# Kernel tuning notes

Measured on AMD Instinct MI355X. Metric: run time of the kernel, lower is better.

## Reference

```python
import jax, jax.numpy as jnp
import numpy as np

BIG = 1e9
EPS_BETA = 1e-6
EPS_BN = 1e-5

N_NODES = 50000
N_EDGES = 800000
IN_DIM = 128
OUT_DIM = 128


def setup_inputs() -> dict:
    key = jax.random.key(0)
    ks = jax.random.split(key, 8)
    h = jax.random.normal(ks[0], (N_NODES, IN_DIM), dtype=jnp.float32)
    src = jax.random.randint(ks[1], (N_EDGES,), 0, N_NODES, dtype=jnp.int32)
    dst = jax.random.randint(ks[2], (N_EDGES,), 0, N_NODES, dtype=jnp.int32)
    sigma_GD = jax.random.uniform(ks[3], (N_EDGES,), dtype=jnp.float32)
    fc_w = jax.random.normal(ks[4], (IN_DIM, OUT_DIM), dtype=jnp.float32) / np.sqrt(IN_DIM)
    fc_b = jax.random.normal(ks[5], (OUT_DIM,), dtype=jnp.float32) * 0.01
    attn_w = jax.random.normal(ks[6], (2 * OUT_DIM, 1), dtype=jnp.float32) / np.sqrt(2 * OUT_DIM)
    attn_b = jax.random.normal(ks[7], (1,), dtype=jnp.float32) * 0.01
    bn_gamma = jnp.ones((OUT_DIM,), dtype=jnp.float32)
    bn_beta = jnp.zeros((OUT_DIM,), dtype=jnp.float32)
    return {"h": h, "src": src, "dst": dst, "sigma_GD": sigma_GD,
            "fc_w": fc_w, "fc_b": fc_b, "attn_w": attn_w, "attn_b": attn_b,
            "bn_gamma": bn_gamma, "bn_beta": bn_beta}


def reference(h, src, dst, sigma_GD, fc_w, fc_b, attn_w, attn_b, bn_gamma, bn_beta):
    n = h.shape[0]
    # node projection
    z = h @ fc_w + fc_b                                   # [N, D]
    z = jnp.where(jnp.isinf(z), BIG, z)
    # per-edge attention logits: concat(src,dst) @ W == src@W1 + dst@W2 (avoid concat materialization)
    d = z.shape[1]
    w_src, w_dst = attn_w[:d], attn_w[d:]
    z_src = z[src]                                        # [E, D]
    a = z_src @ w_src + z[dst] @ w_dst + attn_b           # [E, 1]
    a = jnp.where(jnp.isinf(a), BIG, a)
    e = jax.nn.leaky_relu(a, negative_slope=0.01)[:, 0]   # [E]
    # segment softmax over incoming edges (mailbox softmax)
    m = jax.ops.segment_max(e, dst, num_segments=n)       # [N]
    ex = jnp.exp(e - m[dst])
    denom = jax.ops.segment_sum(ex, dst, num_segments=n)  # [N]
    alpha = ex / denom[dst]                               # [E]
    # beta: sigma_GD normalized per destination node
    bsum = jax.ops.segment_sum(sigma_GD, dst, num_segments=n)
    beta = sigma_GD / (bsum[dst] + EPS_BETA)              # [E]
    # weighted scatter-sum of source features
    h_new = jax.ops.segment_sum((alpha * beta)[:, None] * z_src, dst, num_segments=n)  # [N, D]
    h_new = jnp.where(jnp.isinf(h_new), BIG, h_new)
    # BatchNorm1d (training-mode batch stats, biased variance, as torch does)
    mu = h_new.mean(axis=0)
    var = ((h_new - mu) ** 2).mean(axis=0)
    h_bn = (h_new - mu) * jax.lax.rsqrt(var + EPS_BN) * bn_gamma + bn_beta
    return jax.nn.elu(h_bn)
```

## Files before the change

kernel.cpp:

```cpp
#include <hip/hip_runtime.h>
#include <hip/hip_fp16.h>
#include <math.h>

#define N_NODES 50000
#define N_EDGES 800000
#define BIGV 1000000000.0f
#define NBLK_GEMM 3125
#define CHUNK 1024
#define NCHUNK 782
#define NCH4 784
#define NBUCKET 1563
#define NBK4 1564
#define BMAX 768
#define OVFSTRIDE 1024
#define NBLK_BN 512

typedef _Float16 half8 __attribute__((ext_vector_type(8)));
typedef float floatx4 __attribute__((ext_vector_type(4)));

__device__ __forceinline__ float clampinf(float x) { return isinf(x) ? BIGV : x; }

__device__ __forceinline__ void barrier_lgkm_only() {
    __builtin_amdgcn_sched_barrier(0);
    asm volatile("s_waitcnt lgkmcnt(0)" ::: "memory");
    __builtin_amdgcn_s_barrier();
    __builtin_amdgcn_sched_barrier(0);
}

__global__ __launch_bounds__(256) void k_prep(const float* __restrict__ W,
                                              __half* __restrict__ wt,
                                              float* __restrict__ bns,
                                              const int* __restrict__ dst,
                                              int* __restrict__ countsT)
{
    __shared__ int hist[NBK4];
    const int t = threadIdx.x;
    const int idx = blockIdx.x * 256 + t;
    if (idx < 16384) {
        int n = idx >> 7, k = idx & 127;
        wt[idx] = __float2half(W[k * 128 + n]);
    }
    if (idx < 256) bns[idx] = 0.f;
    for (int i = t; i < NBK4; i += 256) hist[i] = 0;
    __syncthreads();
    const int base = blockIdx.x * CHUNK;
    for (int i = t; i < CHUNK; i += 256) {
        int e = base + i;
        if (e < N_EDGES) atomicAdd(&hist[dst[e] >> 5], 1);
    }
    __syncthreads();
    for (int i = t; i < NBK4; i += 256)
        countsT[(size_t)i * NCH4 + blockIdx.x] = hist[i];
}

__global__ __launch_bounds__(256) void k_off(const int* __restrict__ countsT,
                                             int* __restrict__ cursC,
                                             int* __restrict__ btot)
{
    const int wv = (blockIdx.x << 2) + (threadIdx.x >> 6);
    const int l = threadIdx.x & 63;
    if (wv >= NBUCKET) {
        if (l == 0 && wv < NBK4) btot[wv] = 0;
        return;
    }
    const int* row = countsT + (size_t)wv * NCH4;
    int carry = 0;
    #pragma unroll
    for (int p = 0; p < 13; ++p) {
        const int c = p * 64 + l;
        const int v = (c < NCHUNK) ? row[c] : 0;
        int x = v;
        #pragma unroll
        for (int o = 1; o < 64; o <<= 1) {
            int u = __shfl_up(x, o);
            if (l >= o) x += u;
        }
        if (c < NCHUNK) cursC[(size_t)c * NBK4 + wv] = carry + x - v;
        carry += __shfl(x, 63);
    }
    if (l == 0) btot[wv] = carry;
}

__global__ __launch_bounds__(256) void k_gemm(
    const float* __restrict__ h, const __half* __restrict__ wt,
    const float* __restrict__ bias, const float* __restrict__ attn_w,
    __half* __restrict__ zh, float* __restrict__ sv, float* __restrict__ tv)
{
    __shared__ _Float16 hA[16][136];
    __shared__ float spart[4][16], tpart[4][16];

    const int tid = threadIdx.x;
    const int lane = tid & 63;
    const int wv = tid >> 6;
    const int l16 = lane & 15;
    const int oct = lane >> 4;
    const int n0 = wv << 5;
    const int node0 = blockIdx.x << 4;

    {
        const float4* h4 = (const float4*)(h + (size_t)node0 * 128);
        for (int i = tid; i < 512; i += 256) {
            int r = i >> 5, c4 = i & 31;
            float4 v = h4[i];
            union { __half2 h2[2]; uint2 u; } pk;
            pk.h2[0] = __floats2half2_rn(v.x, v.y);
            pk.h2[1] = __floats2half2_rn(v.z, v.w);
            *(uint2*)&hA[r][c4 << 2] = pk.u;
        }
    }

    half8 bfrag[4][2];
    #pragma unroll
    for (int kk = 0; kk < 4; ++kk)
        #pragma unroll
        for (int t = 0; t < 2; ++t)
            bfrag[kk][t] = *(const half8*)(wt + (size_t)(n0 + t * 16 + l16) * 128
                                              + kk * 32 + oct * 8);

    const float bv0 = bias[n0 + l16],         bv1 = bias[n0 + 16 + l16];
    const float ws0 = attn_w[n0 + l16],       ws1 = attn_w[n0 + 16 + l16];
    const float wd0 = attn_w[128 + n0 + l16], wd1 = attn_w[128 + n0 + 16 + l16];

    barrier_lgkm_only();

    floatx4 acc0 = {0.f, 0.f, 0.f, 0.f};
    floatx4 acc1 = {0.f, 0.f, 0.f, 0.f};
    #pragma unroll
    for (int kk = 0; kk < 4; ++kk) {
        half8 a = *(const half8*)&hA[l16][(kk << 5) + (oct << 3)];
        acc0 = __builtin_amdgcn_mfma_f32_16x16x32_f16(a, bfrag[kk][0], acc0, 0, 0, 0);
        acc1 = __builtin_amdgcn_mfma_f32_16x16x32_f16(a, bfrag[kk][1], acc1, 0, 0, 0);
    }

    float s_acc[4], t_acc[4];
    #pragma unroll
    for (int r = 0; r < 4; ++r) {
        float z0 = clampinf(acc0[r] + bv0);
        float z1 = clampinf(acc1[r] + bv1);
        const int row = (oct << 2) + r;
        zh[(size_t)(node0 + row) * 128 + n0 + l16]      = __float2half(z0);
        zh[(size_t)(node0 + row) * 128 + n0 + 16 + l16] = __float2half(z1);
        s_acc[r] = z0 * ws0 + z1 * ws1;
        t_acc[r] = z0 * wd0 + z1 * wd1;
    }
    #pragma unroll
    for (int r = 0; r < 4; ++r) {
        #pragma unroll
        for (int o = 1; o < 16; o <<= 1) {
            s_acc[r] += __shfl_xor(s_acc[r], o);
            t_acc[r] += __shfl_xor(t_acc[r], o);
        }
    }
    if (l16 == 0) {
        #pragma unroll
        for (int r = 0; r < 4; ++r) {
            spart[wv][(oct << 2) + r] = s_acc[r];
            tpart[wv][(oct << 2) + r] = t_acc[r];
        }
    }
    barrier_lgkm_only();
    if (tid < 16) {
        sv[node0 + tid] = spart[0][tid] + spart[1][tid] + spart[2][tid] + spart[3][tid];
        tv[node0 + tid] = tpart[0][tid] + tpart[1][tid] + tpart[2][tid] + tpart[3][tid];
    }
}

__global__ __launch_bounds__(512) void k_scat(
    const int* __restrict__ src, const int* __restrict__ dst,
    const float* __restrict__ sigma,
    const float* __restrict__ sv, const float* __restrict__ tv,
    const float* __restrict__ attn_b,
    const int* __restrict__ cursC, const int* __restrict__ btot,
    float4* __restrict__ tmp, int* __restrict__ bbase_g)
{
    __shared__ int cur[NBK4];
    __shared__ int bb[NBK4];
    __shared__ int tsc[512];
    const int t = threadIdx.x;
    const int self = blockIdx.x;

    for (int i = t; i < NBK4; i += 512) cur[i] = cursC[(size_t)self * NBK4 + i];

    uint4 bt = {0u, 0u, 0u, 0u};
    int tsum = 0;
    if (t < NBK4 / 4) {
        bt = ((const uint4*)btot)[t];
        tsum = (int)(bt.x + bt.y + bt.z + bt.w);
    }
    tsc[t] = tsum;
    __syncthreads();
    for (int off = 1; off < 512; off <<= 1) {
        int u = (t >= off) ? tsc[t - off] : 0;
        __syncthreads();
        tsc[t] += u;
        __syncthreads();
    }
    if (t < NBK4 / 4) {
        const int v0 = tsc[t] - tsum;
        bb[4*t+0] = v0;
        bb[4*t+1] = v0 + (int)bt.x;
        bb[4*t+2] = v0 + (int)bt.x + (int)bt.y;
        bb[4*t+3] = v0 + (int)bt.x + (int)bt.y + (int)bt.z;
    }
    __syncthreads();
    for (int i = t; i < NBK4; i += 512) cur[i] += bb[i];
    if (self == 0)
        for (int i = t; i < NBK4; i += 512) bbase_g[i] = bb[i];
    __syncthreads();

    const float ab = attn_b[0];
    const int base = self * CHUNK;
    for (int i = t; i < CHUNK; i += 512) {
        int e = base + i;
        if (e < N_EDGES) {
            int s = src[e];
            int d = dst[e];
            float a = sv[s] + tv[d] + ab;
            a = clampinf(a);
            float ev = a > 0.f ? a : 0.01f * a;
            int pos = atomicAdd(&cur[d >> 5], 1);
            float4 rec;
            rec.x = __int_as_float(s);
            rec.y = sigma[e];
            rec.z = ev;
            rec.w = __int_as_float(d);
            tmp[pos] = rec;
        }
    }
}

__global__ __launch_bounds__(512) void k_bagg(
    const float4* __restrict__ tmp, const int* __restrict__ bbase_g,
    const __half* __restrict__ zh, float4* __restrict__ ovf,
    float* __restrict__ out)
{
    __shared__ float4 lrec[BMAX];
    __shared__ int hist[32];
    __shared__ int segs[33];
    __shared__ int cur[32];
    const int t = threadIdx.x;
    const int b = blockIdx.x;
    const int s0 = bbase_g[b];
    const int n  = bbase_g[b + 1] - s0;

    if (t < 32) hist[t] = 0;
    __syncthreads();
    const float* tw = (const float*)tmp;
    for (int i = t; i < n; i += 512) {
        int d = __float_as_int(tw[4 * (size_t)(s0 + i) + 3]);
        atomicAdd(&hist[d & 31], 1);
    }
    __syncthreads();
    if (t < 32) {
        const int hv = hist[t];
        int x = hv;
        #pragma unroll
        for (int o = 1; o < 32; o <<= 1) {
            int u = __shfl_up(x, o);
            if (t >= o) x += u;
        }
        segs[t] = x - hv;
        cur[t]  = x - hv;
        if (t == 31) segs[32] = x;
    }
    __syncthreads();
    for (int i = t; i < n; i += 512) {
        float4 rec = tmp[s0 + i];
        int d = __float_as_int(rec.w);
        int pos = atomicAdd(&cur[d & 31], 1);
        if (pos < BMAX) lrec[pos] = rec;
        else            ovf[(size_t)b * OVFSTRIDE + (pos - BMAX)] = rec;
    }
    __syncthreads();

    const int lane = t & 63;
    const int wv = t >> 6;
    const int grp = lane >> 4;
    const int l16 = lane & 15;

    for (int j = wv; j < 32; j += 8) {
        const int node = (b << 5) + j;
        if (node >= N_NODES) continue;
        const int beg = segs[j];
        const int deg = segs[j + 1] - beg;
        float acc[8] = {0.f,0.f,0.f,0.f,0.f,0.f,0.f,0.f};

        if (deg > 0) {
            if (deg <= 64 && n <= BMAX) {
                int sidx = 0; float sig = 0.f, e = -INFINITY;
                if (lane < deg) {
                    float4 r = lrec[beg + lane];
                    sidx = __float_as_int(r.x); sig = r.y; e = r.z;
                }
                float m = e;
                for (int o = 32; o; o >>= 1) m = fmaxf(m, __shfl_xor(m, o));
                float p = (lane < deg) ? __expf(e - m) : 0.f;
                float dn = p, bs = sig;
                for (int o = 32; o; o >>= 1) {
                    dn += __shfl_xor(dn, o);
                    bs += __shfl_xor(bs, o);
                }
                const float coef = p * sig * (1.0f / dn) / (bs + 1e-6f);
                if (lane < deg) lrec[beg + lane].y = coef;
                const int dm = deg - 1;
                for (int c = 0; c < deg; c += 16) {
                    const int j0 = c + grp, j1 = j0 + 4, j2 = j0 + 8, j3 = j0 + 12;
                    float2 q0 = *(const float2*)&lrec[beg + min(j0, dm)];
                    float2 q1 = *(const float2*)&lrec[beg + min(j1, dm)];
                    float2 q2 = *(const float2*)&lrec[beg + min(j2, dm)];
                    float2 q3 = *(const float2*)&lrec[beg + min(j3, dm)];
                    uint4 r0 = *(const uint4*)(zh + ((size_t)__float_as_int(q0.x) << 7) + (l16 << 3));
                    uint4 r1 = *(const uint4*)(zh + ((size_t)__float_as_int(q1.x) << 7) + (l16 << 3));
                    uint4 r2 = *(const uint4*)(zh + ((size_t)__float_as_int(q2.x) << 7) + (l16 << 3));
                    uint4 r3 = *(const uint4*)(zh + ((size_t)__float_as_int(q3.x) << 7) + (l16 << 3));
                    const float c0 = (j0 < deg) ? q0.y : 0.f;
                    const float c1 = (j1 < deg) ? q1.y : 0.f;
                    const float c2 = (j2 < deg) ? q2.y : 0.f;
                    const float c3 = (j3 < deg) ? q3.y : 0.f;
                    const __half2* h0 = (const __half2*)&r0;
                    const __half2* h1 = (const __half2*)&r1;
                    const __half2* h2 = (const __half2*)&r2;
                    const __half2* h3 = (const __half2*)&r3;
                    #pragma unroll
                    for (int k = 0; k < 4; ++k) {
                        float2 f0 = __half22float2(h0[k]);
                        float2 f1 = __half22float2(h1[k]);
                        float2 f2 = __half22float2(h2[k]);
                        float2 f3 = __half22float2(h3[k]);
                        acc[2*k]   = fmaf(c0, f0.x, acc[2*k]);
                        acc[2*k+1] = fmaf(c0, f0.y, acc[2*k+1]);
                        acc[2*k]   = fmaf(c1, f1.x, acc[2*k]);
                        acc[2*k+1] = fmaf(c1, f1.y, acc[2*k+1]);
                        acc[2*k]   = fmaf(c2, f2.x, acc[2*k]);
                        acc[2*k+1] = fmaf(c2, f2.y, acc[2*k+1]);
                        acc[2*k]   = fmaf(c3, f3.x, acc[2*k]);
                        acc[2*k+1] = fmaf(c3, f3.y, acc[2*k+1]);
                    }
                }
            } else if (deg <= 64) {
                int sidx = 0; float sig = 0.f, e = -INFINITY;
                if (lane < deg) {
                    const int off = beg + lane;
                    float4 r = (off < BMAX) ? lrec[off]
                             : ovf[(size_t)b * OVFSTRIDE + (off - BMAX)];
                    sidx = __float_as_int(r.x); sig = r.y; e = r.z;
                }
                float m = e;
                for (int o = 32; o; o >>= 1) m = fmaxf(m, __shfl_xor(m, o));
                float p = (lane < deg) ? __expf(e - m) : 0.f;
                float dn = p, bs = sig;
                for (int o = 32; o; o >>= 1) {
                    dn += __shfl_xor(dn, o);
                    bs += __shfl_xor(bs, o);
                }
                const float coef = p * sig * (1.0f / dn) / (bs + 1e-6f);
                for (int c = 0; c < deg; c += 4) {
                    const int jj = c + grp;
                    const int js = (jj < deg) ? jj : 0;
                    float cf = __shfl(coef, js);
                    int sj = __shfl(sidx, js);
                    if (jj < deg) {
                        uint4 raw = *(const uint4*)(zh + ((size_t)sj << 7) + (l16 << 3));
                        const __half2* hp = (const __half2*)&raw;
                        #pragma unroll
                        for (int k = 0; k < 4; ++k) {
                            float2 f = __half22float2(hp[k]);
                            acc[2*k]   = fmaf(cf, f.x, acc[2*k]);
                            acc[2*k+1] = fmaf(cf, f.y, acc[2*k+1]);
                        }
                    }
                }
            } else {
                float m = -INFINITY;
                for (int i = lane; i < deg; i += 64) {
                    const int off = beg + i;
                    float4 r = (off < BMAX) ? lrec[off]
                             : ovf[(size_t)b * OVFSTRIDE + (off - BMAX)];
                    m = fmaxf(m, r.z);
                }
                for (int o = 32; o; o >>= 1) m = fmaxf(m, __shfl_xor(m, o));
                float dn = 0.f, bs = 0.f;
                for (int i = lane; i < deg; i += 64) {
                    const int off = beg + i;
                    float4 r = (off < BMAX) ? lrec[off]
                             : ovf[(size_t)b * OVFSTRIDE + (off - BMAX)];
                    dn += __expf(r.z - m); bs += r.y;
                }
                for (int o = 32; o; o >>= 1) {
                    dn += __shfl_xor(dn, o);
                    bs += __shfl_xor(bs, o);
                }
                const float scale = (1.0f / dn) / (bs + 1e-6f);
                for (int c = 0; c < deg; c += 64) {
                    int i = c + lane;
                    int sidx = 0; float coef = 0.f;
                    if (i < deg) {
                        const int off = beg + i;
                        float4 r = (off < BMAX) ? lrec[off]
                                 : ovf[(size_t)b * OVFSTRIDE + (off - BMAX)];
                        sidx = __float_as_int(r.x);
                        coef = __expf(r.z - m) * r.y * scale;
                    }
                    const int cnt2 = min(64, deg - c);
                    for (int jj = 0; jj < cnt2; jj += 4) {
                        const int j4 = jj + grp;
                        const int js = (j4 < cnt2) ? j4 : 0;
                        float cf = __shfl(coef, js);
                        int sj = __shfl(sidx, js);
                        if (j4 < cnt2) {
                            uint4 raw = *(const uint4*)(zh + ((size_t)sj << 7) + (l16 << 3));
                            const __half2* hp = (const __half2*)&raw;
                            #pragma unroll
                            for (int k = 0; k < 4; ++k) {
                                float2 f = __half22float2(hp[k]);
                                acc[2*k]   = fmaf(cf, f.x, acc[2*k]);
                                acc[2*k+1] = fmaf(cf, f.y, acc[2*k+1]);
                            }
                        }
                    }
                }
            }
        }
        #pragma unroll
        for (int k = 0; k < 8; ++k) {
            acc[k] += __shfl_xor(acc[k], 16);
            acc[k] += __shfl_xor(acc[k], 32);
        }
        if (grp == 0) {
            float4 o0, o1;
            o0.x = clampinf(acc[0]); o0.y = clampinf(acc[1]);
            o0.z = clampinf(acc[2]); o0.w = clampinf(acc[3]);
            o1.x = clampinf(acc[4]); o1.y = clampinf(acc[5]);
            o1.z = clampinf(acc[6]); o1.w = clampinf(acc[7]);
            float4* op = (float4*)(out + (size_t)node * 128 + (l16 << 3));
            op[0] = o0; op[1] = o1;
        }
    }
}

__global__ __launch_bounds__(256) void k_bnstats(const float* __restrict__ hnew,
                                                 float* __restrict__ partials)
{
    const int tid = threadIdx.x;
    const int f4 = (tid & 31) << 2;
    const int rgrp = tid >> 5;
    float4 s = {0.f, 0.f, 0.f, 0.f}, q = {0.f, 0.f, 0.f, 0.f};
    for (int node = blockIdx.x * 8 + rgrp; node < N_NODES; node += NBLK_BN * 8) {
        float4 v = *(const float4*)(hnew + (size_t)node * 128 + f4);
        s.x += v.x; s.y += v.y; s.z += v.z; s.w += v.w;
        q.x += v.x * v.x; q.y += v.y * v.y; q.z += v.z * v.z; q.w += v.w * v.w;
    }
    __shared__ float4 ls[256], lq[256];
    ls[tid] = s; lq[tid] = q;
    __syncthreads();
    for (int off = 128; off >= 32; off >>= 1) {
        if (tid < off) {
            float4 a = ls[tid + off], b = lq[tid + off];
            ls[tid].x += a.x; ls[tid].y += a.y; ls[tid].z += a.z; ls[tid].w += a.w;
            lq[tid].x += b.x; lq[tid].y += b.y; lq[tid].z += b.z; lq[tid].w += b.w;
        }
        __syncthreads();
    }
    if (tid < 32) {
        float* p = partials + (size_t)blockIdx.x * 256;
        *(float4*)(p + f4)       = ls[tid];
        *(float4*)(p + 128 + f4) = lq[tid];
    }
}

__global__ __launch_bounds__(1024) void k_bnred(const float* __restrict__ partials,
                                                float* __restrict__ sums)
{
    __shared__ float red[4][256];
    const int t = threadIdx.x;
    const int f = t & 255;
    const int part = t >> 8;
    float s = 0.f;
    #pragma unroll 8
    for (int b = part * (NBLK_BN / 4); b < (part + 1) * (NBLK_BN / 4); ++b)
        s += partials[(size_t)b * 256 + f];
    red[part][f] = s;
    __syncthreads();
    if (part == 0)
        sums[f] = red[0][f] + red[1][f] + red[2][f] + red[3][f];
}

__global__ __launch_bounds__(256) void k_bnapply(float* __restrict__ io,
                                                 const float* __restrict__ sums,
                                                 const float* __restrict__ gamma,
                                                 const float* __restrict__ beta)
{
    __shared__ float sc[128], sh[128];
    const int tid = threadIdx.x;
    if (tid < 128) {
        const float invn = 1.0f / (float)N_NODES;
        float mu = sums[tid] * invn;
        float var = fmaxf(sums[128 + tid] * invn - mu * mu, 0.f);
        float g = gamma[tid] * rsqrtf(var + 1e-5f);
        sc[tid] = g;
        sh[tid] = beta[tid] - mu * g;
    }
    __syncthreads();
    const size_t idx = (size_t)blockIdx.x * 256 + tid;
    const int f4 = ((int)idx & 31) << 2;
    float4 x = ((const float4*)io)[idx];
    float y0 = x.x * sc[f4 + 0] + sh[f4 + 0];
    float y1 = x.y * sc[f4 + 1] + sh[f4 + 1];
    float y2 = x.z * sc[f4 + 2] + sh[f4 + 2];
    float y3 = x.w * sc[f4 + 3] + sh[f4 + 3];
    float4 o;
    o.x = y0 > 0.f ? y0 : expm1f(y0);
    o.y = y1 > 0.f ? y1 : expm1f(y1);
    o.z = y2 > 0.f ? y2 : expm1f(y2);
    o.w = y3 > 0.f ? y3 : expm1f(y3);
    ((float4*)io)[idx] = o;
}

extern "C" void kernel_launch(void* const* d_in, const int* in_sizes, int n_in,
                              void* d_out, int out_size, void* d_ws, size_t ws_size,
                              hipStream_t stream)
{
    const float* h      = (const float*)d_in[0];
    const int*   src    = (const int*)  d_in[1];
    const int*   dst    = (const int*)  d_in[2];
    const float* sigma  = (const float*)d_in[3];
    const float* fc_w   = (const float*)d_in[4];
    const float* fc_b   = (const float*)d_in[5];
    const float* attn_w = (const float*)d_in[6];
    const float* attn_b = (const float*)d_in[7];
    const float* gamma  = (const float*)d_in[8];
    const float* beta   = (const float*)d_in[9];
    float* out = (float*)d_out;

    float4* tmp    = (float4*)d_ws;
    float4* ovf    = tmp + N_EDGES;
    __half* zh     = (__half*)(ovf + (size_t)NBK4 * OVFSTRIDE);
    float*  sv     = (float*)(zh + (size_t)N_NODES * 128);
    float*  tv     = sv + N_NODES;
    float*  bns    = tv + N_NODES;
    float*  parts  = bns + 256;
    __half* wt     = (__half*)(parts + (size_t)NBLK_BN * 256);
    int*    countsT= (int*)(wt + 16384);
    int*    cursC  = countsT + (size_t)NBK4 * NCH4;
    int*    btot   = cursC + (size_t)NCH4 * NBK4;
    int*    bbase  = btot + NBK4;

    k_prep    <<<NCHUNK, 256, 0, stream>>>(fc_w, wt, bns, dst, countsT);
    k_off     <<<NBK4 / 4, 256, 0, stream>>>(countsT, cursC, btot);
    k_gemm    <<<NBLK_GEMM, 256, 0, stream>>>(h, wt, fc_b, attn_w, zh, sv, tv);
    k_scat    <<<NCHUNK, 512, 0, stream>>>(src, dst, sigma, sv, tv, attn_b,
                                           cursC, btot, tmp, bbase);
    k_bagg    <<<NBUCKET, 512, 0, stream>>>(tmp, bbase, zh, ovf, out);
    k_bnstats <<<NBLK_BN, 256, 0, stream>>>(out, parts);
    k_bnred   <<<1, 1024, 0, stream>>>(parts, bns);
    k_bnapply <<<(N_NODES * 128) / (256 * 4), 256, 0, stream>>>(out, bns, gamma, beta);
}
```

Measured before the change: 218.1 us.

## Compute per-node softmax stats with block-wide LDS atomics during bucket scatter

Records are now read once into registers, reused for both the histogram and the scatter pass, which drops the second global read. During the scatter, per-node max (via an ordered int key) and sigma sums are accumulated with LDS atomics. A new block-wide pass computes the exponentials, the denominators and a per-node scale. The per-wave shuffle reductions in the common fast path are removed, and the fast path no longer requires deg<=64. The cost is more LDS atomics and extra barriers, and float atomic summation order becomes nondeterministic.

Result: faster. 208.6 us (-4.4%).

```diff
diff --git a/kernel.cpp b/kernel.cpp
--- a/kernel.cpp
+++ b/kernel.cpp
@@ -19,6 +19,14 @@
 typedef float floatx4 __attribute__((ext_vector_type(4)));
 
 __device__ __forceinline__ float clampinf(float x) { return isinf(x) ? BIGV : x; }
+
+__device__ __forceinline__ int fkey(float x) {
+    int b = __float_as_int(x);
+    return (b >= 0) ? b : (b ^ 0x7FFFFFFF);
+}
+__device__ __forceinline__ float fkey_inv(int k) {
+    return __int_as_float((k >= 0) ? k : (k ^ 0x7FFFFFFF));
+}
 
 __device__ __forceinline__ void barrier_lgkm_only() {
     __builtin_amdgcn_sched_barrier(0);
@@ -238,18 +246,27 @@
     __shared__ int hist[32];
     __shared__ int segs[33];
     __shared__ int cur[32];
+    __shared__ int mkey[32];
+    __shared__ float dnod[32], bsum[32], scale[32];
     const int t = threadIdx.x;
     const int b = blockIdx.x;
     const int s0 = bbase_g[b];
     const int n  = bbase_g[b + 1] - s0;
 
-    if (t < 32) hist[t] = 0;
-    __syncthreads();
-    const float* tw = (const float*)tmp;
-    for (int i = t; i < n; i += 512) {
-        int d = __float_as_int(tw[4 * (size_t)(s0 + i) + 3]);
-        atomicAdd(&hist[d & 31], 1);
-    }
+    if (t < 32) {
+        hist[t] = 0; mkey[t] = (int)0x80000000;
+        dnod[t] = 0.f; bsum[t] = 0.f;
+    }
+    __syncthreads();
+
+    float4 rec0, rec1;
+    const bool h0 = (t < n), h1 = (t + 512 < n);
+    if (h0) rec0 = tmp[s0 + t];
+    if (h1) rec1 = tmp[s0 + t + 512];
+    if (h0) atomicAdd(&hist[__float_as_int(rec0.w) & 31], 1);
+    if (h1) atomicAdd(&hist[__float_as_int(rec1.w) & 31], 1);
+    for (int i = t + 1024; i < n; i += 512)
+        atomicAdd(&hist[__float_as_int(tmp[s0 + i].w) & 31], 1);
     __syncthreads();
     if (t < 32) {
         const int hv = hist[t];
@@ -264,13 +281,44 @@
         if (t == 31) segs[32] = x;
     }
     __syncthreads();
-    for (int i = t; i < n; i += 512) {
+    if (h0) {
+        const int bin = __float_as_int(rec0.w) & 31;
+        int pos = atomicAdd(&cur[bin], 1);
+        if (pos < BMAX) lrec[pos] = rec0;
+        else            ovf[(size_t)b * OVFSTRIDE + (pos - BMAX)] = rec0;
+        atomicAdd(&bsum[bin], rec0.y);
+        atomicMax(&mkey[bin], fkey(rec0.z));
+    }
+    if (h1) {
+        const int bin = __float_as_int(rec1.w) & 31;
+        int pos = atomicAdd(&cur[bin], 1);
+        if (pos < BMAX) lrec[pos] = rec1;
+        else            ovf[(size_t)b * OVFSTRIDE + (pos - BMAX)] = rec1;
+        atomicAdd(&bsum[bin], rec1.y);
+        atomicMax(&mkey[bin], fkey(rec1.z));
+    }
+    for (int i = t + 1024; i < n; i += 512) {
         float4 rec = tmp[s0 + i];
-        int d = __float_as_int(rec.w);
-        int pos = atomicAdd(&cur[d & 31], 1);
+        const int bin = __float_as_int(rec.w) & 31;
+        int pos = atomicAdd(&cur[bin], 1);
         if (pos < BMAX) lrec[pos] = rec;
         else            ovf[(size_t)b * OVFSTRIDE + (pos - BMAX)] = rec;
-    }
+        atomicAdd(&bsum[bin], rec.y);
+        atomicMax(&mkey[bin], fkey(rec.z));
+    }
+    __syncthreads();
+    if (n <= BMAX) {
+        for (int i = t; i < n; i += 512) {
+            float4 r = lrec[i];
+            const int bin = __float_as_int(r.w) & 31;
+            const float m = fkey_inv(mkey[bin]);
+            const float p = __expf(r.z - m);
+            atomicAdd(&dnod[bin], p);
+            lrec[i].w = p * r.y;
+        }
+    }
+    __syncthreads();
+    if (t < 32) scale[t] = (1.0f / dnod[t]) / (bsum[t] + 1e-6f);
     __syncthreads();
 
     const int lane = t & 63;
@@ -286,47 +334,33 @@
         float acc[8] = {0.f,0.f,0.f,0.f,0.f,0.f,0.f,0.f};
 
         if (deg > 0) {
-            if (deg <= 64 && n <= BMAX) {
-                int sidx = 0; float sig = 0.f, e = -INFINITY;
-                if (lane < deg) {
-                    float4 r = lrec[beg + lane];
-                    sidx = __float_as_int(r.x); sig = r.y; e = r.z;
-                }
-                float m = e;
-                for (int o = 32; o; o >>= 1) m = fmaxf(m, __shfl_xor(m, o));
-                float p = (lane < deg) ? __expf(e - m) : 0.f;
-                float dn = p, bs = sig;
-                for (int o = 32; o; o >>= 1) {
-                    dn += __shfl_xor(dn, o);
-                    bs += __shfl_xor(bs, o);
-                }
-                const float coef = p * sig * (1.0f / dn) / (bs + 1e-6f);
-                if (lane < deg) lrec[beg + lane].y = coef;
+            if (n <= BMAX) {
+                const float sc = scale[j];
                 const int dm = deg - 1;
                 for (int c = 0; c < deg; c += 16) {
                     const int j0 = c + grp, j1 = j0 + 4, j2 = j0 + 8, j3 = j0 + 12;
-                    float2 q0 = *(const float2*)&lrec[beg + min(j0, dm)];
-                    float2 q1 = *(const float2*)&lrec[beg + min(j1, dm)];
-                    float2 q2 = *(const float2*)&lrec[beg + min(j2, dm)];
-                    float2 q3 = *(const float2*)&lrec[beg + min(j3, dm)];
+                    float4 q0 = lrec[beg + min(j0, dm)];
+                    float4 q1 = lrec[beg + min(j1, dm)];
+                    float4 q2 = lrec[beg + min(j2, dm)];
+                    float4 q3 = lrec[beg + min(j3, dm)];
                     uint4 r0 = *(const uint4*)(zh + ((size_t)__float_as_int(q0.x) << 7) + (l16 << 3));
                     uint4 r1 = *(const uint4*)(zh + ((size_t)__float_as_int(q1.x) << 7) + (l16 << 3));
                     uint4 r2 = *(const uint4*)(zh + ((size_t)__float_as_int(q2.x) << 7) + (l16 << 3));
                     uint4 r3 = *(const uint4*)(zh + ((size_t)__float_as_int(q3.x) << 7) + (l16 << 3));
-                    const float c0 = (j0 < deg) ? q0.y : 0.f;
-                    const float c1 = (j1 < deg) ? q1.y : 0.f;
-                    const float c2 = (j2 < deg) ? q2.y : 0.f;
-                    const float c3 = (j3 < deg) ? q3.y : 0.f;
-                    const __half2* h0 = (const __half2*)&r0;
-                    const __half2* h1 = (const __half2*)&r1;
-                    const __half2* h2 = (const __half2*)&r2;
-                    const __half2* h3 = (const __half2*)&r3;
+                    const float c0 = (j0 < deg) ? q0.w * sc : 0.f;
+                    const float c1 = (j1 < deg) ? q1.w * sc : 0.f;
+                    const float c2 = (j2 < deg) ? q2.w * sc : 0.f;
+                    const float c3 = (j3 < deg) ? q3.w * sc : 0.f;
+                    const __half2* h0p = (const __half2*)&r0;
+                    const __half2* h1p = (const __half2*)&r1;
+                    const __half2* h2p = (const __half2*)&r2;
+                    const __half2* h3p = (const __half2*)&r3;
                     #pragma unroll
                     for (int k = 0; k < 4; ++k) {
-                        float2 f0 = __half22float2(h0[k]);
-                        float2 f1 = __half22float2(h1[k]);
-                        float2 f2 = __half22float2(h2[k]);
-                        float2 f3 = __half22float2(h3[k]);
+                        float2 f0 = __half22float2(h0p[k]);
+                        float2 f1 = __half22float2(h1p[k]);
+                        float2 f2 = __half22float2(h2p[k]);
+                        float2 f3 = __half22float2(h3p[k]);
                         acc[2*k]   = fmaf(c0, f0.x, acc[2*k]);
                         acc[2*k+1] = fmaf(c0, f0.y, acc[2*k+1]);
                         acc[2*k]   = fmaf(c1, f1.x, acc[2*k]);
@@ -390,7 +424,7 @@
                     dn += __shfl_xor(dn, o);
                     bs += __shfl_xor(bs, o);
                 }
-                const float scale = (1.0f / dn) / (bs + 1e-6f);
+                const float scl = (1.0f / dn) / (bs + 1e-6f);
                 for (int c = 0; c < deg; c += 64) {
                     int i = c + lane;
                     int sidx = 0; float coef = 0.f;
@@ -399,7 +433,7 @@
                         float4 r = (off < BMAX) ? lrec[off]
                                  : ovf[(size_t)b * OVFSTRIDE + (off - BMAX)];
                         sidx = __float_as_int(r.x);
-                        coef = __expf(r.z - m) * r.y * scale;
+                        coef = __expf(r.z - m) * r.y * scl;
                     }
                     const int cnt2 = min(64, deg - c);
                     for (int jj = 0; jj < cnt2; jj += 4) {
```
